# Optimization experiments

Hardware: AMD Instinct MI355X
Metric: run time of the kernel (lower is better)

Reference implementation:

```python
import jax, jax.numpy as jnp
import numpy as np


def setup_inputs() -> dict:
    key = jax.random.key(0)
    img = jax.random.uniform(key, (3, 4096, 4096), dtype=jnp.float32)
    return {"img": img, "param": 500}


def reference(img, param):
    # Original: poissonNoise = np.random.poisson(param, img.shape).astype(float)
    #           noisy = img + poissonNoise
    noise_key = jax.random.fold_in(jax.random.key(0), 1)
    noise = jax.random.poisson(noise_key, float(param), shape=img.shape).astype(img.dtype)
    return img + noise
```

## Files before the change

### kernel.cpp

```cpp
#include <hip/hip_runtime.h>
#include <stdint.h>
#include <math.h>


#pragma clang fp contract(off)

#define TOTAL_ELEMS 50331648u
#define N_BLOCKS    2048
#define N_TPB       256
#define TOTAL_THREADS 524288u
#define ELEMS_PER_THREAD 96
#define CAP 32
#define TAB_LO 256
#define TAB_N  512
#define QCAP 3072
#define CHUNK_J 4
#define AQ_CAP 384
#define LOG_LAM ((float)6.2146080984221914)

__device__ __forceinline__ uint32_t rotl32(uint32_t v, uint32_t r) {
  return (v << r) | (v >> (32u - r));
}

__device__ __forceinline__ void tf2x32(uint32_t k0, uint32_t k1,
                                       uint32_t c0, uint32_t c1,
                                       uint32_t& o0, uint32_t& o1) {
  uint32_t ks2 = k0 ^ k1 ^ 0x1BD11BDAu;
  uint32_t x0 = c0 + k0;
  uint32_t x1 = c1 + k1;
#define TF_R(r) { x0 += x1; x1 = rotl32(x1, r); x1 ^= x0; }
  TF_R(13u) TF_R(15u) TF_R(26u) TF_R(6u)
  x0 += k1;  x1 += ks2 + 1u;
  TF_R(17u) TF_R(29u) TF_R(16u) TF_R(24u)
  x0 += ks2; x1 += k0 + 2u;
  TF_R(13u) TF_R(15u) TF_R(26u) TF_R(6u)
  x0 += k0;  x1 += k1 + 3u;
  TF_R(17u) TF_R(29u) TF_R(16u) TF_R(24u)
  x0 += k1;  x1 += ks2 + 4u;
  TF_R(13u) TF_R(15u) TF_R(26u) TF_R(6u)
  x0 += ks2; x1 += k0 + 5u;
#undef TF_R
  o0 = x0; o1 = x1;
}

__device__ __forceinline__ float xla_logf(float xin) {
  #pragma clang fp contract(off)
  if (xin == 0.0f) return -__builtin_inff();
  if (!(xin > 0.0f)) return __builtin_nanf("");
  float x = fmaxf(xin, __uint_as_float(0x00800000u));
  uint32_t ix = __float_as_uint(x);
  float e = 1.0f + (float)((int32_t)(ix >> 23) - 127);
  x = __uint_as_float((ix & 0x807fffffu) | 0x3f000000u);
  const float SQRTHF = (float)0.707106781186547524;
  bool m = x < SQRTHF;
  float tmp1 = m ? x : 0.0f;
  x = x - 1.0f;
  e = e - (m ? 1.0f : 0.0f);
  x = x + tmp1;
  float x2 = x * x;
  float x3 = x2 * x;
  float y  = __builtin_fmaf(x, (float)7.0376836292e-2,  (float)-1.1514610310e-1);
  float y1 = __builtin_fmaf(x, (float)-1.2420140846e-1, (float)1.4249322787e-1);
  float y2 = __builtin_fmaf(x, (float)2.0000714765e-1,  (float)-2.4999993993e-1);
  y  = __builtin_fmaf(y,  x, (float)1.1676998740e-1);
  y1 = __builtin_fmaf(y1, x, (float)-1.6668057665e-1);
  y2 = __builtin_fmaf(y2, x, (float)3.3333331174e-1);
  y  = __builtin_fmaf(y, x3, y1);
  y  = __builtin_fmaf(y, x3, y2);
  float yq1 = (float)-2.12194440e-4 * e;
  y = __builtin_fmaf(y, x3, yq1);
  x = __builtin_fmaf(-0.5f, x2, x);
  x = x + y;
  x = __builtin_fmaf((float)0.693359375, e, x);
  return x;
}

__device__ __forceinline__ float xla_log1pf(float x) {
  #pragma clang fp contract(off)
  float for_small = __builtin_fmaf(-0.5f, x, 1.0f) * x;
  float for_large = xla_logf(x + 1.0f);
  return (fabsf(x) < (float)1e-4) ? for_small : for_large;
}

__device__ __forceinline__ float xla_lgammaf(float a) {
  #pragma clang fp contract(off)
  float z = a - 1.0f;
  float sum = (float)0.99999999999980993227684700473478;
  sum = sum + (float)676.520368121885098567009190444019   / (z + 1.0f);
  sum = sum + (float)-1259.13921672240287047156078755283  / (z + 2.0f);
  sum = sum + (float)771.3234287776530788486528258894     / (z + 3.0f);
  sum = sum + (float)-176.61502916214059906584551354      / (z + 4.0f);
  sum = sum + (float)12.507343278686904814458936853       / (z + 5.0f);
  sum = sum + (float)-0.13857109526572011689554707        / (z + 6.0f);
  sum = sum + (float)9.984369578019570859563e-6           / (z + 7.0f);
  sum = sum + (float)1.50563273514931155834e-7            / (z + 8.0f);
  float t = (float)7.5 + z;
  float w = z * (float)(1.0 / 7.5);
  float log_t = (float)2.0149030205422647 + xla_log1pf(w);
  float factor = (z + 0.5f) - t / log_t;
  float log_y = __builtin_fmaf(factor, log_t, (float)0.91893853320467274178)
                + xla_logf(sum);
  return log_y;
}

__device__ __forceinline__ float t_of_k(float k) {
  #pragma clang fp contract(off)
  return __builtin_fmaf(k, LOG_LAM, -500.0f) - xla_lgammaf(k + 1.0f);
}

struct PC { float bb, aa, twoa, inv_alpha, v_r; };

__device__ __forceinline__ PC make_pc() {
  #pragma clang fp contract(off)
  PC c;
  float sq = (float)22.360679774997896;
  c.bb = (float)0.931 + (float)2.53 * sq;
  c.aa = (float)-0.059 + (float)0.02483 * c.bb;
  c.twoa = 2.0f * c.aa;
  c.inv_alpha = (float)1.1239 + (float)1.1328 / (c.bb - (float)3.4);
  c.v_r = (float)0.9277 - (float)3.6224 / (c.bb - 2.0f);
  return c;
}

__device__ __forceinline__ float bits_to_u01(uint32_t bits) {
  return __uint_as_float((bits >> 9) | 0x3f800000u) - 1.0f;
}

__device__ __forceinline__ float t_lookup(float k, const float* __restrict__ ttab) {
  int ki = (int)k;
  if (ki >= TAB_LO && ki < TAB_LO + TAB_N) return ttab[ki - TAB_LO];
  return t_of_k(k);
}

__device__ __forceinline__ bool hormann_accept(uint32_t ubits, uint32_t vbits,
                                               const PC& c, const float* __restrict__ ttab,
                                               float& kout) {
  #pragma clang fp contract(off)
  float u01 = bits_to_u01(ubits);
  float v   = bits_to_u01(vbits);
  float u = u01 - 0.5f;
  float us = 0.5f - fabsf(u);
  float inner = c.twoa / us + c.bb;
  float kq = __builtin_fmaf(inner, u, 500.43f);
  float k = floorf(kq);
  kout = k;
  bool accept1 = (us >= (float)0.07) & (v <= c.v_r);
  if (accept1) return true;
  bool reject = (k < 0.0f) | ((us < (float)0.013) & (v > us));
  if (reject) return false;
  float s = xla_logf((v * c.inv_alpha) / (c.aa / (us * us) + c.bb));
  return s <= t_lookup(k, ttab);
}

__device__ __forceinline__ uint32_t pbits(uint32_t s0, uint32_t s1, uint32_t e) {
  uint32_t a, b;
  tf2x32(s0, s1, 0u, e, a, b);
  return a ^ b;
}

__device__ __forceinline__ bool trial(uint32_t e, uint32_t tlvl,
                                      const uint32_t (&ssub)[CAP][4],
                                      const PC& c, const float* __restrict__ ttab,
                                      float& kout) {
  uint32_t ub = pbits(ssub[tlvl][0], ssub[tlvl][1], e);
  uint32_t vb = pbits(ssub[tlvl][2], ssub[tlvl][3], e);
  return hormann_accept(ub, vb, c, ttab, kout);
}

__device__ __forceinline__ uint32_t lane_id() {
  return __builtin_amdgcn_mbcnt_hi(~0u, __builtin_amdgcn_mbcnt_lo(~0u, 0u));
}

__device__ __forceinline__ uint32_t wq_push(uint32_t* counter, bool push) {
  uint64_t mask = __ballot(push);
  if (mask == 0ull) return 0xFFFFFFFFu;
  uint32_t lane = lane_id();
  int leader = (int)(__ffsll((unsigned long long)mask) - 1);
  uint32_t base = 0;
  if ((int)lane == leader) base = atomicAdd(counter, (uint32_t)__popcll(mask));
  base = (uint32_t)__shfl((int)base, leader);
  uint32_t off = (uint32_t)__popcll(mask & ((1ull << lane) - 1ull));
  return base + off;
}

__device__ __forceinline__ void build_shared(uint32_t n, uint32_t (&ssub)[CAP][4],
                                             float* ttab) {
  for (uint32_t i = threadIdx.x; i < TAB_N; i += N_TPB) {
    ttab[i] = t_of_k((float)(int)(TAB_LO + (int)i));
  }
  if (threadIdx.x == 0) {
    uint32_t k0, k1;
    tf2x32(0u, 0u, 0u, 1u, k0, k1);
    for (uint32_t t = 0; t < n; ++t) {
      uint32_t nk0, nk1, s00, s01, s10, s11;
      tf2x32(k0, k1, 0u, 0u, nk0, nk1);
      tf2x32(k0, k1, 0u, 1u, s00, s01);
      tf2x32(k0, k1, 0u, 2u, s10, s11);
      ssub[t][0] = s00; ssub[t][1] = s01;
      ssub[t][2] = s10; ssub[t][3] = s11;
      k0 = nk0; k1 = nk1;
    }
  }
  __syncthreads();
}

__global__ void pn_init(uint32_t* nmax) { *nmax = 0u; }

__global__ __launch_bounds__(N_TPB) void pn_pass1(uint32_t* nmax) {
  __shared__ uint32_t ssub[CAP][4];
  __shared__ float ttab[TAB_N];
  __shared__ uint16_t qf[2][QCAP];
  __shared__ uint32_t qn[2];
  __shared__ uint32_t shN;
  __shared__ uint16_t aq_li[AQ_CAP];
  __shared__ float aq_u[AQ_CAP];
  __shared__ float aq_v[AQ_CAP];
  __shared__ uint32_t aqn;
  if (threadIdx.x == 0) { qn[0] = 0; qn[1] = 0; shN = 1; }
  build_shared(CAP, ssub, ttab);
  PC c = make_pc();
  uint32_t blockBase = blockIdx.x * N_TPB;
  for (int jc = 0; jc < ELEMS_PER_THREAD; jc += CHUNK_J) {
    if (threadIdx.x == 0) aqn = 0;
    __syncthreads();
    for (int j = jc; j < jc + CHUNK_J; ++j) {
      uint32_t e = blockBase + threadIdx.x + (uint32_t)j * TOTAL_THREADS;
      uint16_t li = (uint16_t)(((uint32_t)j << 8) | threadIdx.x);
      uint32_t ub = pbits(ssub[0][0], ssub[0][1], e);
      uint32_t vb = pbits(ssub[0][2], ssub[0][3], e);
      float u01 = bits_to_u01(ub);
      float v   = bits_to_u01(vb);
      float u = u01 - 0.5f;
      float us = 0.5f - fabsf(u);
      bool accept1 = (us >= (float)0.07) & (v <= c.v_r);
      bool pend = !accept1;
      uint32_t ai = wq_push(&aqn, pend);
      if (pend) {
        if (__builtin_expect(ai < AQ_CAP, 1)) {
          aq_li[ai] = li; aq_u[ai] = u; aq_v[ai] = v;
        } else {
          float inner = c.twoa / us + c.bb;
          float k = floorf(__builtin_fmaf(inner, u, 500.43f));
          bool reject = (k < 0.0f) | ((us < (float)0.013) & (v > us));
          bool acc = false;
          if (!reject) {
            float s = xla_logf((v * c.inv_alpha) / (c.aa / (us * us) + c.bb));
            acc = (s <= t_lookup(k, ttab));
          }
          if (!acc) {
            uint32_t qi = atomicAdd(&qn[0], 1u);
            if (qi < QCAP) qf[0][qi] = li;
            else {
              float kk; uint32_t Lc = CAP;
              for (uint32_t t2 = 1; t2 < CAP; ++t2)
                if (trial(e, t2, ssub, c, ttab, kk)) { Lc = t2 + 1u; break; }
              atomicMax(&shN, Lc);
            }
          }
        }
      }
    }
    __syncthreads();
    uint32_t an = aqn; if (an > AQ_CAP) an = AQ_CAP;
    for (uint32_t i = threadIdx.x; i < an; i += N_TPB) {
      uint16_t li = aq_li[i];
      float u = aq_u[i], v = aq_v[i];
      float us = 0.5f - fabsf(u);
      float inner = c.twoa / us + c.bb;
      float k = floorf(__builtin_fmaf(inner, u, 500.43f));
      bool reject = (k < 0.0f) | ((us < (float)0.013) & (v > us));
      bool acc = false;
      if (!reject) {
        float s = xla_logf((v * c.inv_alpha) / (c.aa / (us * us) + c.bb));
        acc = (s <= t_lookup(k, ttab));
      }
      bool fail = !acc;
      uint32_t qi = wq_push(&qn[0], fail);
      if (fail) {
        if (__builtin_expect(qi < QCAP, 1)) qf[0][qi] = li;
        else {
          uint32_t e = blockBase + (li & 255u) + (uint32_t)(li >> 8) * TOTAL_THREADS;
          float kk; uint32_t Lc = CAP;
          for (uint32_t t2 = 1; t2 < CAP; ++t2)
            if (trial(e, t2, ssub, c, ttab, kk)) { Lc = t2 + 1u; break; }
          atomicMax(&shN, Lc);
        }
      }
    }
    __syncthreads();
  }
  int cur = 0;
  uint32_t localN = 1;
  for (uint32_t t = 1; t < CAP; ++t) {
    uint32_t n = qn[cur]; if (n > QCAP) n = QCAP;
    if (n == 0) break;
    localN = t + 1u;
    if (threadIdx.x == 0) qn[cur ^ 1] = 0;
    __syncthreads();
    for (uint32_t i = threadIdx.x; i < n; i += N_TPB) {
      uint16_t li = qf[cur][i];
      uint32_t e = blockBase + (li & 255u) + (uint32_t)(li >> 8) * TOTAL_THREADS;
      float kk;
      bool fail = !trial(e, t, ssub, c, ttab, kk);
      uint32_t qi = wq_push(&qn[cur ^ 1], fail);
      if (fail) {
        if (__builtin_expect(qi < QCAP, 1)) qf[cur ^ 1][qi] = li;
        else {
          uint32_t Lc = CAP;
          for (uint32_t t2 = t + 1; t2 < CAP; ++t2)
            if (trial(e, t2, ssub, c, ttab, kk)) { Lc = t2 + 1u; break; }
          atomicMax(&shN, Lc);
        }
      }
    }
    __syncthreads();
    cur ^= 1;
  }
  __syncthreads();
  if (threadIdx.x == 0) {
    uint32_t m = shN; if (localN > m) m = localN;
    atomicMax(nmax, m);
  }
}

__global__ __launch_bounds__(N_TPB) void pn_pass2(const float* __restrict__ img,
                                                  float* __restrict__ out,
                                                  const uint32_t* __restrict__ nptr) {
  __shared__ uint32_t ssub[CAP][4];
  __shared__ float ttab[TAB_N];
  __shared__ uint16_t qf[2][QCAP];
  __shared__ uint32_t qn[2];
  __shared__ uint16_t aq_li[AQ_CAP];
  __shared__ float aq_k[AQ_CAP];
  __shared__ float aq_us[AQ_CAP];
  __shared__ float aq_v[AQ_CAP];
  __shared__ uint32_t aqn;
  uint32_t N = *nptr;
  if (N < 1u) N = 1u;
  if (N > CAP) N = CAP;
  if (threadIdx.x == 0) { qn[0] = 0; qn[1] = 0; }
  build_shared(N, ssub, ttab);
  PC c = make_pc();
  uint32_t blockBase = blockIdx.x * N_TPB;
  uint32_t top = N - 1u;
  for (int jc = 0; jc < ELEMS_PER_THREAD; jc += CHUNK_J) {
    if (threadIdx.x == 0) aqn = 0;
    __syncthreads();
    for (int j = jc; j < jc + CHUNK_J; ++j) {
      uint32_t e = blockBase + threadIdx.x + (uint32_t)j * TOTAL_THREADS;
      uint16_t li = (uint16_t)(((uint32_t)j << 8) | threadIdx.x);
      uint32_t ub = pbits(ssub[top][0], ssub[top][1], e);
      uint32_t vb = pbits(ssub[top][2], ssub[top][3], e);
      float u01 = bits_to_u01(ub);
      float v   = bits_to_u01(vb);
      float u = u01 - 0.5f;
      float us = 0.5f - fabsf(u);
      float inner = c.twoa / us + c.bb;
      float k = floorf(__builtin_fmaf(inner, u, 500.43f));
      bool accept1 = (us >= (float)0.07) & (v <= c.v_r);
      bool reject  = (!accept1) & ((k < 0.0f) | ((us < (float)0.013) & (v > us)));
      bool need2   = (!accept1) & (!reject);
      if (accept1) out[e] = img[e] + k;
      uint32_t qi = wq_push(&qn[0], reject);
      if (reject) {
        if (__builtin_expect(qi < QCAP, 1)) qf[0][qi] = li;
        else {
          float kk, kf = -1.0f;
          for (int t2 = (int)top - 1; t2 >= 0; --t2)
            if (trial(e, (uint32_t)t2, ssub, c, ttab, kk)) { kf = kk; break; }
          out[e] = img[e] + kf;
        }
      }
      uint32_t ai = wq_push(&aqn, need2);
      if (need2) {
        if (__builtin_expect(ai < AQ_CAP, 1)) {
          aq_li[ai] = li; aq_k[ai] = k; aq_us[ai] = us; aq_v[ai] = v;
        } else {
          float s = xla_logf((v * c.inv_alpha) / (c.aa / (us * us) + c.bb));
          if (s <= t_lookup(k, ttab)) out[e] = img[e] + k;
          else {
            uint32_t qi2 = atomicAdd(&qn[0], 1u);
            if (qi2 < QCAP) qf[0][qi2] = li;
            else {
              float kk, kf = -1.0f;
              for (int t2 = (int)top - 1; t2 >= 0; --t2)
                if (trial(e, (uint32_t)t2, ssub, c, ttab, kk)) { kf = kk; break; }
              out[e] = img[e] + kf;
            }
          }
        }
      }
    }
    __syncthreads();
    uint32_t an = aqn; if (an > AQ_CAP) an = AQ_CAP;
    for (uint32_t i = threadIdx.x; i < an; i += N_TPB) {
      uint16_t li = aq_li[i];
      float k = aq_k[i], us = aq_us[i], v = aq_v[i];
      uint32_t e = blockBase + (li & 255u) + (uint32_t)(li >> 8) * TOTAL_THREADS;
      float s = xla_logf((v * c.inv_alpha) / (c.aa / (us * us) + c.bb));
      bool acc = (s <= t_lookup(k, ttab));
      if (acc) out[e] = img[e] + k;
      uint32_t qi = wq_push(&qn[0], !acc);
      if (!acc) {
        if (__builtin_expect(qi < QCAP, 1)) qf[0][qi] = li;
        else {
          float kk, kf = -1.0f;
          for (int t2 = (int)top - 1; t2 >= 0; --t2)
            if (trial(e, (uint32_t)t2, ssub, c, ttab, kk)) { kf = kk; break; }
          out[e] = img[e] + kf;
        }
      }
    }
    __syncthreads();
  }
  int cur = 0;
  for (int t = (int)top - 1; t >= 0; --t) {
    uint32_t n = qn[cur]; if (n > QCAP) n = QCAP;
    if (n == 0) break;
    if (threadIdx.x == 0) qn[cur ^ 1] = 0;
    __syncthreads();
    for (uint32_t i = threadIdx.x; i < n; i += N_TPB) {
      uint16_t li = qf[cur][i];
      uint32_t e = blockBase + (li & 255u) + (uint32_t)(li >> 8) * TOTAL_THREADS;
      float kk;
      bool acc = trial(e, (uint32_t)t, ssub, c, ttab, kk);
      if (acc) out[e] = img[e] + kk;
      uint32_t qi = wq_push(&qn[cur ^ 1], !acc);
      if (!acc) {
        if (__builtin_expect(qi < QCAP, 1)) qf[cur ^ 1][qi] = li;
        else {
          float kk2, kf = -1.0f;
          for (int t2 = t - 1; t2 >= 0; --t2)
            if (trial(e, (uint32_t)t2, ssub, c, ttab, kk2)) { kf = kk2; break; }
          out[e] = img[e] + kf;
        }
      }
    }
    __syncthreads();
    cur ^= 1;
  }
  uint32_t n = qn[cur]; if (n > QCAP) n = QCAP;
  for (uint32_t i = threadIdx.x; i < n; i += N_TPB) {
    uint16_t li = qf[cur][i];
    uint32_t e = blockBase + (li & 255u) + (uint32_t)(li >> 8) * TOTAL_THREADS;
    out[e] = img[e] - 1.0f;
  }
}

extern "C" void kernel_launch(void* const* d_in, const int* in_sizes, int n_in,
                              void* d_out, int out_size, void* d_ws, size_t ws_size,
                              hipStream_t stream) {
  (void)in_sizes; (void)n_in; (void)out_size; (void)ws_size;
  const float* img = (const float*)d_in[0];
  float* out = (float*)d_out;
  uint32_t* nmax = (uint32_t*)d_ws;
  pn_init<<<1, 1, 0, stream>>>(nmax);
  pn_pass1<<<N_BLOCKS, N_TPB, 0, stream>>>(nmax);
  pn_pass2<<<N_BLOCKS, N_TPB, 0, stream>>>(img, out, nmax);
}
```

Baseline: 802.5 us.

## Resolve retry queues per chunk and write outputs once via shared staging

```diff
diff --git a/kernel.cpp b/kernel.cpp
--- a/kernel.cpp
+++ b/kernel.cpp
@@ -13,8 +13,8 @@
 #define CAP 32
 #define TAB_LO 256
 #define TAB_N  512
-#define QCAP 3072
 #define CHUNK_J 4
+#define QCAP2 256
 #define AQ_CAP 384
 #define LOG_LAM ((float)6.2146080984221914)
 
@@ -209,19 +209,20 @@
 __global__ __launch_bounds__(N_TPB) void pn_pass1(uint32_t* nmax) {
   __shared__ uint32_t ssub[CAP][4];
   __shared__ float ttab[TAB_N];
-  __shared__ uint16_t qf[2][QCAP];
+  __shared__ uint16_t qf[2][QCAP2];
   __shared__ uint32_t qn[2];
   __shared__ uint32_t shN;
   __shared__ uint16_t aq_li[AQ_CAP];
   __shared__ float aq_u[AQ_CAP];
   __shared__ float aq_v[AQ_CAP];
   __shared__ uint32_t aqn;
-  if (threadIdx.x == 0) { qn[0] = 0; qn[1] = 0; shN = 1; }
+  if (threadIdx.x == 0) shN = 1;
   build_shared(CAP, ssub, ttab);
   PC c = make_pc();
   uint32_t blockBase = blockIdx.x * N_TPB;
+  uint32_t localN = 1;
   for (int jc = 0; jc < ELEMS_PER_THREAD; jc += CHUNK_J) {
-    if (threadIdx.x == 0) aqn = 0;
+    if (threadIdx.x == 0) { aqn = 0; qn[0] = 0; qn[1] = 0; }
     __syncthreads();
     for (int j = jc; j < jc + CHUNK_J; ++j) {
       uint32_t e = blockBase + threadIdx.x + (uint32_t)j * TOTAL_THREADS;
@@ -249,7 +250,7 @@
           }
           if (!acc) {
             uint32_t qi = atomicAdd(&qn[0], 1u);
-            if (qi < QCAP) qf[0][qi] = li;
+            if (qi < QCAP2) qf[0][qi] = li;
             else {
               float kk; uint32_t Lc = CAP;
               for (uint32_t t2 = 1; t2 < CAP; ++t2)
@@ -277,7 +278,7 @@
       bool fail = !acc;
       uint32_t qi = wq_push(&qn[0], fail);
       if (fail) {
-        if (__builtin_expect(qi < QCAP, 1)) qf[0][qi] = li;
+        if (__builtin_expect(qi < QCAP2, 1)) qf[0][qi] = li;
         else {
           uint32_t e = blockBase + (li & 255u) + (uint32_t)(li >> 8) * TOTAL_THREADS;
           float kk; uint32_t Lc = CAP;
@@ -288,35 +289,34 @@
       }
     }
     __syncthreads();
+    int cur = 0;
+    for (uint32_t t = 1; t < CAP; ++t) {
+      uint32_t n = qn[cur]; if (n > QCAP2) n = QCAP2;
+      if (n == 0) break;
+      if (localN < t + 1u) localN = t + 1u;
+      if (threadIdx.x == 0) qn[cur ^ 1] = 0;
+      __syncthreads();
+      for (uint32_t i = threadIdx.x; i < n; i += N_TPB) {
+        uint16_t li = qf[cur][i];
+        uint32_t e = blockBase + (li & 255u) + (uint32_t)(li >> 8) * TOTAL_THREADS;
+        float kk;
+        bool fail = !trial(e, t, ssub, c, ttab, kk);
+        uint32_t qi = wq_push(&qn[cur ^ 1], fail);
+        if (fail) {
+          if (__builtin_expect(qi < QCAP2, 1)) qf[cur ^ 1][qi] = li;
+          else {
+            uint32_t Lc = CAP;
+            for (uint32_t t2 = t + 1; t2 < CAP; ++t2)
+              if (trial(e, t2, ssub, c, ttab, kk)) { Lc = t2 + 1u; break; }
+            atomicMax(&shN, Lc);
+          }
+        }
+      }
+      __syncthreads();
+      cur ^= 1;
+    }
+    __syncthreads();
   }
-  int cur = 0;
-  uint32_t localN = 1;
-  for (uint32_t t = 1; t < CAP; ++t) {
-    uint32_t n = qn[cur]; if (n > QCAP) n = QCAP;
-    if (n == 0) break;
-    localN = t + 1u;
-    if (threadIdx.x == 0) qn[cur ^ 1] = 0;
-    __syncthreads();
-    for (uint32_t i = threadIdx.x; i < n; i += N_TPB) {
-      uint16_t li = qf[cur][i];
-      uint32_t e = blockBase + (li & 255u) + (uint32_t)(li >> 8) * TOTAL_THREADS;
-      float kk;
-      bool fail = !trial(e, t, ssub, c, ttab, kk);
-      uint32_t qi = wq_push(&qn[cur ^ 1], fail);
-      if (fail) {
-        if (__builtin_expect(qi < QCAP, 1)) qf[cur ^ 1][qi] = li;
-        else {
-          uint32_t Lc = CAP;
-          for (uint32_t t2 = t + 1; t2 < CAP; ++t2)
-            if (trial(e, t2, ssub, c, ttab, kk)) { Lc = t2 + 1u; break; }
-          atomicMax(&shN, Lc);
-        }
-      }
-    }
-    __syncthreads();
-    cur ^= 1;
-  }
-  __syncthreads();
   if (threadIdx.x == 0) {
     uint32_t m = shN; if (localN > m) m = localN;
     atomicMax(nmax, m);
@@ -328,27 +328,29 @@
                                                   const uint32_t* __restrict__ nptr) {
   __shared__ uint32_t ssub[CAP][4];
   __shared__ float ttab[TAB_N];
-  __shared__ uint16_t qf[2][QCAP];
+  __shared__ uint16_t qf[2][QCAP2];
   __shared__ uint32_t qn[2];
   __shared__ uint16_t aq_li[AQ_CAP];
   __shared__ float aq_k[AQ_CAP];
   __shared__ float aq_us[AQ_CAP];
   __shared__ float aq_v[AQ_CAP];
   __shared__ uint32_t aqn;
+  __shared__ float karr[N_TPB * CHUNK_J];
   uint32_t N = *nptr;
   if (N < 1u) N = 1u;
   if (N > CAP) N = CAP;
-  if (threadIdx.x == 0) { qn[0] = 0; qn[1] = 0; }
   build_shared(N, ssub, ttab);
   PC c = make_pc();
   uint32_t blockBase = blockIdx.x * N_TPB;
   uint32_t top = N - 1u;
   for (int jc = 0; jc < ELEMS_PER_THREAD; jc += CHUNK_J) {
-    if (threadIdx.x == 0) aqn = 0;
+    if (threadIdx.x == 0) { aqn = 0; qn[0] = 0; qn[1] = 0; }
     __syncthreads();
     for (int j = jc; j < jc + CHUNK_J; ++j) {
+      int lj = j - jc;
       uint32_t e = blockBase + threadIdx.x + (uint32_t)j * TOTAL_THREADS;
       uint16_t li = (uint16_t)(((uint32_t)j << 8) | threadIdx.x);
+      uint32_t ci = (uint32_t)lj * N_TPB + threadIdx.x;
       uint32_t ub = pbits(ssub[top][0], ssub[top][1], e);
       uint32_t vb = pbits(ssub[top][2], ssub[top][3], e);
       float u01 = bits_to_u01(ub);
@@ -360,15 +362,15 @@
       bool accept1 = (us >= (float)0.07) & (v <= c.v_r);
       bool reject  = (!accept1) & ((k < 0.0f) | ((us < (float)0.013) & (v > us)));
       bool need2   = (!accept1) & (!reject);
-      if (accept1) out[e] = img[e] + k;
+      karr[ci] = accept1 ? k : -1.0f;
       uint32_t qi = wq_push(&qn[0], reject);
       if (reject) {
-        if (__builtin_expect(qi < QCAP, 1)) qf[0][qi] = li;
+        if (__builtin_expect(qi < QCAP2, 1)) qf[0][qi] = li;
         else {
           float kk, kf = -1.0f;
           for (int t2 = (int)top - 1; t2 >= 0; --t2)
             if (trial(e, (uint32_t)t2, ssub, c, ttab, kk)) { kf = kk; break; }
-          out[e] = img[e] + kf;
+          karr[ci] = kf;
         }
       }
       uint32_t ai = wq_push(&aqn, need2);
@@ -377,15 +379,15 @@
           aq_li[ai] = li; aq_k[ai] = k; aq_us[ai] = us; aq_v[ai] = v;
         } else {
           float s = xla_logf((v * c.inv_alpha) / (c.aa / (us * us) + c.bb));
-          if (s <= t_lookup(k, ttab)) out[e] = img[e] + k;
+          if (s <= t_lookup(k, ttab)) karr[ci] = k;
           else {
             uint32_t qi2 = atomicAdd(&qn[0], 1u);
-            if (qi2 < QCAP) qf[0][qi2] = li;
+            if (qi2 < QCAP2) qf[0][qi2] = li;
             else {
               float kk, kf = -1.0f;
               for (int t2 = (int)top - 1; t2 >= 0; --t2)
                 if (trial(e, (uint32_t)t2, ssub, c, ttab, kk)) { kf = kk; break; }
-              out[e] = img[e] + kf;
+              karr[ci] = kf;
             }
           }
         }
@@ -396,54 +398,58 @@
     for (uint32_t i = threadIdx.x; i < an; i += N_TPB) {
       uint16_t li = aq_li[i];
       float k = aq_k[i], us = aq_us[i], v = aq_v[i];
-      uint32_t e = blockBase + (li & 255u) + (uint32_t)(li >> 8) * TOTAL_THREADS;
+      uint32_t ci = ((uint32_t)(li >> 8) - (uint32_t)jc) * N_TPB + (li & 255u);
       float s = xla_logf((v * c.inv_alpha) / (c.aa / (us * us) + c.bb));
       bool acc = (s <= t_lookup(k, ttab));
-      if (acc) out[e] = img[e] + k;
+      if (acc) karr[ci] = k;
       uint32_t qi = wq_push(&qn[0], !acc);
       if (!acc) {
-        if (__builtin_expect(qi < QCAP, 1)) qf[0][qi] = li;
+        if (__builtin_expect(qi < QCAP2, 1)) qf[0][qi] = li;
         else {
+          uint32_t e = blockBase + (li & 255u) + (uint32_t)(li >> 8) * TOTAL_THREADS;
           float kk, kf = -1.0f;
           for (int t2 = (int)top - 1; t2 >= 0; --t2)
             if (trial(e, (uint32_t)t2, ssub, c, ttab, kk)) { kf = kk; break; }
-          out[e] = img[e] + kf;
-        }
-      }
-    }
-    __syncthreads();
-  }
-  int cur = 0;
-  for (int t = (int)top - 1; t >= 0; --t) {
-    uint32_t n = qn[cur]; if (n > QCAP) n = QCAP;
-    if (n == 0) break;
-    if (threadIdx.x == 0) qn[cur ^ 1] = 0;
-    __syncthreads();
-    for (uint32_t i = threadIdx.x; i < n; i += N_TPB) {
-      uint16_t li = qf[cur][i];
-      uint32_t e = blockBase + (li & 255u) + (uint32_t)(li >> 8) * TOTAL_THREADS;
-      float kk;
-      bool acc = trial(e, (uint32_t)t, ssub, c, ttab, kk);
-      if (acc) out[e] = img[e] + kk;
-      uint32_t qi = wq_push(&qn[cur ^ 1], !acc);
-      if (!acc) {
-        if (__builtin_expect(qi < QCAP, 1)) qf[cur ^ 1][qi] = li;
-        else {
-          float kk2, kf = -1.0f;
-          for (int t2 = t - 1; t2 >= 0; --t2)
-            if (trial(e, (uint32_t)t2, ssub, c, ttab, kk2)) { kf = kk2; break; }
-          out[e] = img[e] + kf;
-        }
-      }
-    }
-    __syncthreads();
-    cur ^= 1;
-  }
-  uint32_t n = qn[cur]; if (n > QCAP) n = QCAP;
-  for (uint32_t i = threadIdx.x; i < n; i += N_TPB) {
-    uint16_t li = qf[cur][i];
-    uint32_t e = blockBase + (li & 255u) + (uint32_t)(li >> 8) * TOTAL_THREADS;
-    out[e] = img[e] - 1.0f;
+          karr[ci] = kf;
+        }
+      }
+    }
+    __syncthreads();
+    int cur = 0;
+    for (int t = (int)top - 1; t >= 0; --t) {
+      uint32_t n = qn[cur]; if (n > QCAP2) n = QCAP2;
+      if (n == 0) break;
+      if (threadIdx.x == 0) qn[cur ^ 1] = 0;
+      __syncthreads();
+      for (uint32_t i = threadIdx.x; i < n; i += N_TPB) {
+        uint16_t li = qf[cur][i];
+        uint32_t e = blockBase + (li & 255u) + (uint32_t)(li >> 8) * TOTAL_THREADS;
+        uint32_t ci = ((uint32_t)(li >> 8) - (uint32_t)jc) * N_TPB + (li & 255u);
+        float kk;
+        bool acc = trial(e, (uint32_t)t, ssub, c, ttab, kk);
+        if (acc) karr[ci] = kk;
+        uint32_t qi = wq_push(&qn[cur ^ 1], !acc);
+        if (!acc) {
+          if (__builtin_expect(qi < QCAP2, 1)) qf[cur ^ 1][qi] = li;
+          else {
+            float kk2, kf = -1.0f;
+            for (int t2 = t - 1; t2 >= 0; --t2)
+              if (trial(e, (uint32_t)t2, ssub, c, ttab, kk2)) { kf = kk2; break; }
+            karr[ci] = kf;
+          }
+        }
+      }
+      __syncthreads();
+      cur ^= 1;
+    }
+    __syncthreads();
+    for (int j = jc; j < jc + CHUNK_J; ++j) {
+      int lj = j - jc;
+      uint32_t e = blockBase + threadIdx.x + (uint32_t)j * TOTAL_THREADS;
+      uint32_t ci = (uint32_t)lj * N_TPB + threadIdx.x;
+      out[e] = img[e] + karr[ci];
+    }
+    __syncthreads();
   }
 }
 
```

After: 958.1 us. +19.4%, slower.

## Replace block-wide compaction queues with per-wave local queues and drop barriers

Applied to the files above, without the earlier changes.

```diff
diff --git a/kernel.cpp b/kernel.cpp
--- a/kernel.cpp
+++ b/kernel.cpp
@@ -11,11 +11,12 @@
 #define TOTAL_THREADS 524288u
 #define ELEMS_PER_THREAD 96
 #define CAP 32
-#define TAB_LO 256
-#define TAB_N  512
+#define TAB_LO 320
+#define TAB_N  384
 #define QCAP 3072
-#define CHUNK_J 4
-#define AQ_CAP 384
+#define CHUNK_J 8
+#define WAQ_CAP 176
+#define NWAVES 4
 #define LOG_LAM ((float)6.2146080984221914)
 
 __device__ __forceinline__ uint32_t rotl32(uint32_t v, uint32_t r) {
@@ -183,6 +184,14 @@
   return base + off;
 }
 
+__device__ __forceinline__ uint32_t wl_push(uint32_t& cnt, bool push) {
+  uint64_t mask = __ballot(push);
+  uint32_t lane = lane_id();
+  uint32_t off = cnt + (uint32_t)__popcll(mask & ((1ull << lane) - 1ull));
+  cnt += (uint32_t)__popcll(mask);
+  return off;
+}
+
 __device__ __forceinline__ void build_shared(uint32_t n, uint32_t (&ssub)[CAP][4],
                                              float* ttab) {
   for (uint32_t i = threadIdx.x; i < TAB_N; i += N_TPB) {
@@ -212,69 +221,93 @@
   __shared__ uint16_t qf[2][QCAP];
   __shared__ uint32_t qn[2];
   __shared__ uint32_t shN;
-  __shared__ uint16_t aq_li[AQ_CAP];
-  __shared__ float aq_u[AQ_CAP];
-  __shared__ float aq_v[AQ_CAP];
-  __shared__ uint32_t aqn;
+  __shared__ uint16_t wli[NWAVES][WAQ_CAP];
+  __shared__ float wu[NWAVES][WAQ_CAP];
+  __shared__ float wv[NWAVES][WAQ_CAP];
   if (threadIdx.x == 0) { qn[0] = 0; qn[1] = 0; shN = 1; }
   build_shared(CAP, ssub, ttab);
   PC c = make_pc();
   uint32_t blockBase = blockIdx.x * N_TPB;
+  uint32_t wid = threadIdx.x >> 6;
+  uint32_t wcnt = 0;
   for (int jc = 0; jc < ELEMS_PER_THREAD; jc += CHUNK_J) {
-    if (threadIdx.x == 0) aqn = 0;
-    __syncthreads();
-    for (int j = jc; j < jc + CHUNK_J; ++j) {
-      uint32_t e = blockBase + threadIdx.x + (uint32_t)j * TOTAL_THREADS;
-      uint16_t li = (uint16_t)(((uint32_t)j << 8) | threadIdx.x);
-      uint32_t ub = pbits(ssub[0][0], ssub[0][1], e);
-      uint32_t vb = pbits(ssub[0][2], ssub[0][3], e);
-      float u01 = bits_to_u01(ub);
-      float v   = bits_to_u01(vb);
-      float u = u01 - 0.5f;
-      float us = 0.5f - fabsf(u);
-      bool accept1 = (us >= (float)0.07) & (v <= c.v_r);
-      bool pend = !accept1;
-      uint32_t ai = wq_push(&aqn, pend);
-      if (pend) {
-        if (__builtin_expect(ai < AQ_CAP, 1)) {
-          aq_li[ai] = li; aq_u[ai] = u; aq_v[ai] = v;
-        } else {
-          float inner = c.twoa / us + c.bb;
-          float k = floorf(__builtin_fmaf(inner, u, 500.43f));
-          bool reject = (k < 0.0f) | ((us < (float)0.013) & (v > us));
+    for (int j = jc; j < jc + CHUNK_J; j += 2) {
+      uint32_t eA = blockBase + threadIdx.x + (uint32_t)j * TOTAL_THREADS;
+      uint32_t eB = eA + TOTAL_THREADS;
+      uint16_t liA = (uint16_t)(((uint32_t)j << 8) | threadIdx.x);
+      uint16_t liB = (uint16_t)liA + (uint16_t)256;
+      uint32_t ubA = pbits(ssub[0][0], ssub[0][1], eA);
+      uint32_t vbA = pbits(ssub[0][2], ssub[0][3], eA);
+      uint32_t ubB = pbits(ssub[0][0], ssub[0][1], eB);
+      uint32_t vbB = pbits(ssub[0][2], ssub[0][3], eB);
+      float uA = bits_to_u01(ubA) - 0.5f, vA = bits_to_u01(vbA);
+      float uB = bits_to_u01(ubB) - 0.5f, vB = bits_to_u01(vbB);
+      float usA = 0.5f - fabsf(uA), usB = 0.5f - fabsf(uB);
+      bool pendA = !((usA >= (float)0.07) & (vA <= c.v_r));
+      bool pendB = !((usB >= (float)0.07) & (vB <= c.v_r));
+      uint32_t oA = wl_push(wcnt, pendA);
+      if (pendA) {
+        if (__builtin_expect(oA < WAQ_CAP, 1)) { wli[wid][oA]=liA; wu[wid][oA]=uA; wv[wid][oA]=vA; }
+        else {
+          float inner = c.twoa / usA + c.bb;
+          float k = floorf(__builtin_fmaf(inner, uA, 500.43f));
+          bool rej = (k < 0.0f) | ((usA < (float)0.013) & (vA > usA));
           bool acc = false;
-          if (!reject) {
-            float s = xla_logf((v * c.inv_alpha) / (c.aa / (us * us) + c.bb));
+          if (!rej) {
+            float s = xla_logf((vA * c.inv_alpha) / (c.aa / (usA * usA) + c.bb));
             acc = (s <= t_lookup(k, ttab));
           }
           if (!acc) {
             uint32_t qi = atomicAdd(&qn[0], 1u);
-            if (qi < QCAP) qf[0][qi] = li;
-            else {
-              float kk; uint32_t Lc = CAP;
+            if (qi < QCAP) qf[0][qi] = liA;
+            else { float kk; uint32_t Lc = CAP;
               for (uint32_t t2 = 1; t2 < CAP; ++t2)
-                if (trial(e, t2, ssub, c, ttab, kk)) { Lc = t2 + 1u; break; }
-              atomicMax(&shN, Lc);
-            }
+                if (trial(eA, t2, ssub, c, ttab, kk)) { Lc = t2 + 1u; break; }
+              atomicMax(&shN, Lc); }
           }
         }
       }
-    }
-    __syncthreads();
-    uint32_t an = aqn; if (an > AQ_CAP) an = AQ_CAP;
-    for (uint32_t i = threadIdx.x; i < an; i += N_TPB) {
-      uint16_t li = aq_li[i];
-      float u = aq_u[i], v = aq_v[i];
+      uint32_t oB = wl_push(wcnt, pendB);
+      if (pendB) {
+        if (__builtin_expect(oB < WAQ_CAP, 1)) { wli[wid][oB]=liB; wu[wid][oB]=uB; wv[wid][oB]=vB; }
+        else {
+          float inner = c.twoa / usB + c.bb;
+          float k = floorf(__builtin_fmaf(inner, uB, 500.43f));
+          bool rej = (k < 0.0f) | ((usB < (float)0.013) & (vB > usB));
+          bool acc = false;
+          if (!rej) {
+            float s = xla_logf((vB * c.inv_alpha) / (c.aa / (usB * usB) + c.bb));
+            acc = (s <= t_lookup(k, ttab));
+          }
+          if (!acc) {
+            uint32_t qi = atomicAdd(&qn[0], 1u);
+            if (qi < QCAP) qf[0][qi] = liB;
+            else { float kk; uint32_t Lc = CAP;
+              for (uint32_t t2 = 1; t2 < CAP; ++t2)
+                if (trial(eB, t2, ssub, c, ttab, kk)) { Lc = t2 + 1u; break; }
+              atomicMax(&shN, Lc); }
+          }
+        }
+      }
+    }
+    uint32_t n = wcnt < WAQ_CAP ? wcnt : WAQ_CAP;
+    uint32_t lane = threadIdx.x & 63u;
+    for (uint32_t base = 0; base < n; base += 64u) {
+      uint32_t i = base + lane;
+      bool live = (i < n);
+      uint16_t li = live ? wli[wid][i] : (uint16_t)0;
+      float u = live ? wu[wid][i] : 0.1f;
+      float v = live ? wv[wid][i] : 0.0f;
       float us = 0.5f - fabsf(u);
       float inner = c.twoa / us + c.bb;
       float k = floorf(__builtin_fmaf(inner, u, 500.43f));
-      bool reject = (k < 0.0f) | ((us < (float)0.013) & (v > us));
+      bool rej = (k < 0.0f) | ((us < (float)0.013) & (v > us));
       bool acc = false;
-      if (!reject) {
+      if (live & !rej) {
         float s = xla_logf((v * c.inv_alpha) / (c.aa / (us * us) + c.bb));
         acc = (s <= t_lookup(k, ttab));
       }
-      bool fail = !acc;
+      bool fail = live & !acc;
       uint32_t qi = wq_push(&qn[0], fail);
       if (fail) {
         if (__builtin_expect(qi < QCAP, 1)) qf[0][qi] = li;
@@ -287,8 +320,9 @@
         }
       }
     }
-    __syncthreads();
-  }
+    wcnt = 0;
+  }
+  __syncthreads();
   int cur = 0;
   uint32_t localN = 1;
   for (uint32_t t = 1; t < CAP; ++t) {
@@ -330,11 +364,10 @@
   __shared__ float ttab[TAB_N];
   __shared__ uint16_t qf[2][QCAP];
   __shared__ uint32_t qn[2];
-  __shared__ uint16_t aq_li[AQ_CAP];
-  __shared__ float aq_k[AQ_CAP];
-  __shared__ float aq_us[AQ_CAP];
-  __shared__ float aq_v[AQ_CAP];
-  __shared__ uint32_t aqn;
+  __shared__ uint16_t wli[NWAVES][WAQ_CAP];
+  __shared__ uint16_t wk[NWAVES][WAQ_CAP];
+  __shared__ float wus[NWAVES][WAQ_CAP];
+  __shared__ float wv[NWAVES][WAQ_CAP];
   uint32_t N = *nptr;
   if (N < 1u) N = 1u;
   if (N > CAP) N = CAP;
@@ -343,76 +376,104 @@
   PC c = make_pc();
   uint32_t blockBase = blockIdx.x * N_TPB;
   uint32_t top = N - 1u;
+  uint32_t wid = threadIdx.x >> 6;
+  uint32_t wcnt = 0;
   for (int jc = 0; jc < ELEMS_PER_THREAD; jc += CHUNK_J) {
-    if (threadIdx.x == 0) aqn = 0;
-    __syncthreads();
-    for (int j = jc; j < jc + CHUNK_J; ++j) {
-      uint32_t e = blockBase + threadIdx.x + (uint32_t)j * TOTAL_THREADS;
-      uint16_t li = (uint16_t)(((uint32_t)j << 8) | threadIdx.x);
-      uint32_t ub = pbits(ssub[top][0], ssub[top][1], e);
-      uint32_t vb = pbits(ssub[top][2], ssub[top][3], e);
-      float u01 = bits_to_u01(ub);
-      float v   = bits_to_u01(vb);
-      float u = u01 - 0.5f;
-      float us = 0.5f - fabsf(u);
-      float inner = c.twoa / us + c.bb;
-      float k = floorf(__builtin_fmaf(inner, u, 500.43f));
-      bool accept1 = (us >= (float)0.07) & (v <= c.v_r);
-      bool reject  = (!accept1) & ((k < 0.0f) | ((us < (float)0.013) & (v > us)));
-      bool need2   = (!accept1) & (!reject);
-      if (accept1) out[e] = img[e] + k;
-      uint32_t qi = wq_push(&qn[0], reject);
-      if (reject) {
+    for (int j = jc; j < jc + CHUNK_J; j += 2) {
+      uint32_t eA = blockBase + threadIdx.x + (uint32_t)j * TOTAL_THREADS;
+      uint32_t eB = eA + TOTAL_THREADS;
+      uint16_t liA = (uint16_t)(((uint32_t)j << 8) | threadIdx.x);
+      uint16_t liB = (uint16_t)liA + (uint16_t)256;
+      uint32_t ubA = pbits(ssub[top][0], ssub[top][1], eA);
+      uint32_t vbA = pbits(ssub[top][2], ssub[top][3], eA);
+      uint32_t ubB = pbits(ssub[top][0], ssub[top][1], eB);
+      uint32_t vbB = pbits(ssub[top][2], ssub[top][3], eB);
+      float uA = bits_to_u01(ubA) - 0.5f, vA = bits_to_u01(vbA);
+      float uB = bits_to_u01(ubB) - 0.5f, vB = bits_to_u01(vbB);
+      float usA = 0.5f - fabsf(uA), usB = 0.5f - fabsf(uB);
+      float kA = floorf(__builtin_fmaf(c.twoa / usA + c.bb, uA, 500.43f));
+      float kB = floorf(__builtin_fmaf(c.twoa / usB + c.bb, uB, 500.43f));
+      bool a1A = (usA >= (float)0.07) & (vA <= c.v_r);
+      bool a1B = (usB >= (float)0.07) & (vB <= c.v_r);
+      bool rjA = (!a1A) & ((kA < 0.0f) | ((usA < (float)0.013) & (vA > usA)));
+      bool rjB = (!a1B) & ((kB < 0.0f) | ((usB < (float)0.013) & (vB > usB)));
+      bool n2A = (!a1A) & (!rjA);
+      bool n2B = (!a1B) & (!rjB);
+      if (a1A) out[eA] = img[eA] + kA;
+      if (a1B) out[eB] = img[eB] + kB;
+      uint32_t qiA = wq_push(&qn[0], rjA);
+      if (rjA) {
+        if (__builtin_expect(qiA < QCAP, 1)) qf[0][qiA] = liA;
+        else { float kk, kf = -1.0f;
+          for (int t2 = (int)top - 1; t2 >= 0; --t2)
+            if (trial(eA, (uint32_t)t2, ssub, c, ttab, kk)) { kf = kk; break; }
+          out[eA] = img[eA] + kf; }
+      }
+      uint32_t qiB = wq_push(&qn[0], rjB);
+      if (rjB) {
+        if (__builtin_expect(qiB < QCAP, 1)) qf[0][qiB] = liB;
+        else { float kk, kf = -1.0f;
+          for (int t2 = (int)top - 1; t2 >= 0; --t2)
+            if (trial(eB, (uint32_t)t2, ssub, c, ttab, kk)) { kf = kk; break; }
+          out[eB] = img[eB] + kf; }
+      }
+      uint32_t oA = wl_push(wcnt, n2A);
+      if (n2A) {
+        if (__builtin_expect(oA < WAQ_CAP, 1)) {
+          wli[wid][oA]=liA; wk[wid][oA]=(uint16_t)(int)kA; wus[wid][oA]=usA; wv[wid][oA]=vA;
+        } else {
+          float s = xla_logf((vA * c.inv_alpha) / (c.aa / (usA * usA) + c.bb));
+          if (s <= t_lookup(kA, ttab)) out[eA] = img[eA] + kA;
+          else { uint32_t qi2 = atomicAdd(&qn[0], 1u);
+            if (qi2 < QCAP) qf[0][qi2] = liA;
+            else { float kk, kf = -1.0f;
+              for (int t2 = (int)top - 1; t2 >= 0; --t2)
+                if (trial(eA, (uint32_t)t2, ssub, c, ttab, kk)) { kf = kk; break; }
+              out[eA] = img[eA] + kf; } }
+        }
+      }
+      uint32_t oB = wl_push(wcnt, n2B);
+      if (n2B) {
+        if (__builtin_expect(oB < WAQ_CAP, 1)) {
+          wli[wid][oB]=liB; wk[wid][oB]=(uint16_t)(int)kB; wus[wid][oB]=usB; wv[wid][oB]=vB;
+        } else {
+          float s = xla_logf((vB * c.inv_alpha) / (c.aa / (usB * usB) + c.bb));
+          if (s <= t_lookup(kB, ttab)) out[eB] = img[eB] + kB;
+          else { uint32_t qi2 = atomicAdd(&qn[0], 1u);
+            if (qi2 < QCAP) qf[0][qi2] = liB;
+            else { float kk, kf = -1.0f;
+              for (int t2 = (int)top - 1; t2 >= 0; --t2)
+                if (trial(eB, (uint32_t)t2, ssub, c, ttab, kk)) { kf = kk; break; }
+              out[eB] = img[eB] + kf; } }
+        }
+      }
+    }
+    uint32_t n = wcnt < WAQ_CAP ? wcnt : WAQ_CAP;
+    uint32_t lane = threadIdx.x & 63u;
+    for (uint32_t base = 0; base < n; base += 64u) {
+      uint32_t i = base + lane;
+      bool live = (i < n);
+      uint16_t li = live ? wli[wid][i] : (uint16_t)0;
+      float k  = live ? (float)(int)wk[wid][i] : 500.0f;
+      float us = live ? wus[wid][i] : 0.1f;
+      float v  = live ? wv[wid][i] : 0.0f;
+      uint32_t e = blockBase + (li & 255u) + (uint32_t)(li >> 8) * TOTAL_THREADS;
+      float s = xla_logf((v * c.inv_alpha) / (c.aa / (us * us) + c.bb));
+      bool acc = live & (s <= t_lookup(k, ttab));
+      if (acc) out[e] = img[e] + k;
+      bool fail = live & !acc;
+      uint32_t qi = wq_push(&qn[0], fail);
+      if (fail) {
         if (__builtin_expect(qi < QCAP, 1)) qf[0][qi] = li;
-        else {
-          float kk, kf = -1.0f;
+        else { float kk, kf = -1.0f;
           for (int t2 = (int)top - 1; t2 >= 0; --t2)
             if (trial(e, (uint32_t)t2, ssub, c, ttab, kk)) { kf = kk; break; }
-          out[e] = img[e] + kf;
-        }
-      }
-      uint32_t ai = wq_push(&aqn, need2);
-      if (need2) {
-        if (__builtin_expect(ai < AQ_CAP, 1)) {
-          aq_li[ai] = li; aq_k[ai] = k; aq_us[ai] = us; aq_v[ai] = v;
-        } else {
-          float s = xla_logf((v * c.inv_alpha) / (c.aa / (us * us) + c.bb));
-          if (s <= t_lookup(k, ttab)) out[e] = img[e] + k;
-          else {
-            uint32_t qi2 = atomicAdd(&qn[0], 1u);
-            if (qi2 < QCAP) qf[0][qi2] = li;
-            else {
-              float kk, kf = -1.0f;
-              for (int t2 = (int)top - 1; t2 >= 0; --t2)
-                if (trial(e, (uint32_t)t2, ssub, c, ttab, kk)) { kf = kk; break; }
-              out[e] = img[e] + kf;
-            }
-          }
-        }
-      }
-    }
-    __syncthreads();
-    uint32_t an = aqn; if (an > AQ_CAP) an = AQ_CAP;
-    for (uint32_t i = threadIdx.x; i < an; i += N_TPB) {
-      uint16_t li = aq_li[i];
-      float k = aq_k[i], us = aq_us[i], v = aq_v[i];
-      uint32_t e = blockBase + (li & 255u) + (uint32_t)(li >> 8) * TOTAL_THREADS;
-      float s = xla_logf((v * c.inv_alpha) / (c.aa / (us * us) + c.bb));
-      bool acc = (s <= t_lookup(k, ttab));
-      if (acc) out[e] = img[e] + k;
-      uint32_t qi = wq_push(&qn[0], !acc);
-      if (!acc) {
-        if (__builtin_expect(qi < QCAP, 1)) qf[0][qi] = li;
-        else {
-          float kk, kf = -1.0f;
-          for (int t2 = (int)top - 1; t2 >= 0; --t2)
-            if (trial(e, (uint32_t)t2, ssub, c, ttab, kk)) { kf = kk; break; }
-          out[e] = img[e] + kf;
-        }
-      }
-    }
-    __syncthreads();
-  }
+          out[e] = img[e] + kf; }
+      }
+    }
+    wcnt = 0;
+  }
+  __syncthreads();
   int cur = 0;
   for (int t = (int)top - 1; t >= 0; --t) {
     uint32_t n = qn[cur]; if (n > QCAP) n = QCAP;
@@ -428,12 +489,10 @@
       uint32_t qi = wq_push(&qn[cur ^ 1], !acc);
       if (!acc) {
         if (__builtin_expect(qi < QCAP, 1)) qf[cur ^ 1][qi] = li;
-        else {
-          float kk2, kf = -1.0f;
+        else { float kk2, kf = -1.0f;
           for (int t2 = t - 1; t2 >= 0; --t2)
             if (trial(e, (uint32_t)t2, ssub, c, ttab, kk2)) { kf = kk2; break; }
-          out[e] = img[e] + kf;
-        }
+          out[e] = img[e] + kf; }
       }
     }
     __syncthreads();
```

After: 755.2 us. 1.06x faster.
